# Kernel optimization log

Hardware: AMD Instinct MI355X
Metric: run time of the kernel (lower is better)

Reference implementation:

```python
import jax, jax.numpy as jnp
import numpy as np

B, S, D = 16, 1024, 768

def setup_inputs() -> dict:
    key = jax.random.key(0)
    k1, k2, k3, k4 = jax.random.split(key, 4)
    head = jax.random.normal(k1, (B, S, D), dtype=jnp.float32)
    dep = jax.random.normal(k2, (B, S, D), dtype=jnp.float32)
    edge_W = jax.random.normal(k3, (1, 2 * D), dtype=jnp.float32)
    edge_b = jax.random.normal(k4, (1,), dtype=jnp.float32)
    return {"head": head, "dep": dep, "edge_W": edge_W, "edge_b": edge_b}

def reference(head, dep, edge_W, edge_b):
    # Original: scores[b,i,j] = edge_W @ concat(head[b,i], dep[b,j]) + edge_b
    # Separable: split W into head-half and dep-half, broadcast-add over grid.
    d = head.shape[-1]
    w_h = edge_W[0, :d]   # [D]
    w_d = edge_W[0, d:]   # [D]
    s_h = jnp.einsum('bid,d->bi', head, w_h)  # [B,S]
    s_d = jnp.einsum('bjd,d->bj', dep, w_d)   # [B,S]
    return s_h[:, :, None] + s_d[:, None, :] + edge_b[0]  # [B,S,S]
```

## Files before the change

kernel.cpp:

```cpp
#include <hip/hip_runtime.h>
#include <hip/hip_bf16.h>


#define B_SZ 16
#define S_SZ 1024
#define D_SZ 768
#define ROWS (B_SZ * S_SZ)

typedef float fx4 __attribute__((ext_vector_type(4)));

__global__ __launch_bounds__(256) void dots_kernel(
    const float* __restrict__ head,
    const float* __restrict__ dep,
    const float* __restrict__ edge_W,
    float* __restrict__ s)
{
    const int gw   = (blockIdx.x * 256 + threadIdx.x) >> 6;
    const int lane = threadIdx.x & 63;
    const int is_dep = gw >> 12;
    const int base   = (gw & 4095) << 2;

    const float* __restrict__ src = is_dep ? dep : head;
    const fx4* __restrict__ wv =
        reinterpret_cast<const fx4*>(edge_W + (is_dep ? D_SZ : 0));

    const fx4 w0 = wv[lane], w1 = wv[lane + 64], w2 = wv[lane + 128];

    float acc[4];
#pragma unroll
    for (int k = 0; k < 4; ++k) {
        const fx4* __restrict__ p =
            reinterpret_cast<const fx4*>(src + (size_t)(base + k) * D_SZ);
        fx4 a0 = p[lane], a1 = p[lane + 64], a2 = p[lane + 128];
        acc[k] = a0.x * w0.x + a0.y * w0.y + a0.z * w0.z + a0.w * w0.w
               + a1.x * w1.x + a1.y * w1.y + a1.z * w1.z + a1.w * w1.w
               + a2.x * w2.x + a2.y * w2.y + a2.z * w2.z + a2.w * w2.w;
    }

#pragma unroll
    for (int k = 0; k < 4; ++k)
#pragma unroll
        for (int off = 32; off; off >>= 1)
            acc[k] += __shfl_down(acc[k], off, 64);

    if (lane == 0) {
        fx4 o; o.x = acc[0]; o.y = acc[1]; o.z = acc[2]; o.w = acc[3];
        *reinterpret_cast<fx4*>(s + (is_dep ? ROWS : 0) + base) = o;
    }
}

__global__ __launch_bounds__(256) void bcast_kernel(
    const float* __restrict__ s,
    const float* __restrict__ edge_b,
    float* __restrict__ out)
{
    const int row0 = blockIdx.x << 4;
    const int b    = row0 >> 10;

    fx4 sd = reinterpret_cast<const fx4*>(s + ROWS + ((size_t)b << 10))[threadIdx.x];
    const float bias = edge_b[0];
    sd.x += bias; sd.y += bias; sd.z += bias; sd.w += bias;

#pragma unroll
    for (int k = 0; k < 16; ++k) {
        const float sh = s[row0 + k];
        fx4 o;
        o.x = sh + sd.x;
        o.y = sh + sd.y;
        o.z = sh + sd.z;
        o.w = sh + sd.w;
        fx4* dst = reinterpret_cast<fx4*>(out + ((size_t)(row0 + k) << 10));
        __builtin_nontemporal_store(o, &dst[threadIdx.x]);
    }
}

extern "C" void kernel_launch(void* const* d_in, const int* in_sizes, int n_in,
                              void* d_out, int out_size, void* d_ws, size_t ws_size,
                              hipStream_t stream) {
    const float* head   = (const float*)d_in[0];
    const float* dep    = (const float*)d_in[1];
    const float* edge_W = (const float*)d_in[2];
    const float* edge_b = (const float*)d_in[3];
    float* out = (float*)d_out;
    float* s   = (float*)d_ws;

    dots_kernel<<<2048, 256, 0, stream>>>(head, dep, edge_W, s);
    bcast_kernel<<<ROWS / 16, 256, 0, stream>>>(s, edge_b, out);
}
```

Baseline: 31.82 us.

## Fuse head dot products into broadcast kernel, keep separate dep dot kernel

Moves the head-row dot products out of the first kernel and into the broadcast kernel. Each block now computes its 16 head scores into shared memory before writing its output rows. The first kernel shrinks to the dep half only, and the broadcast kernel no longer round-trips the head scores through the workspace. The cost is that the broadcast kernel now reads head (about 50 MB) before storing, plus a block-wide sync, which may lengthen its critical path.

```diff
diff --git a/kernel.cpp b/kernel.cpp
--- a/kernel.cpp
+++ b/kernel.cpp
@@ -9,28 +9,23 @@
 
 typedef float fx4 __attribute__((ext_vector_type(4)));
 
-__global__ __launch_bounds__(256) void dots_kernel(
-    const float* __restrict__ head,
+__global__ __launch_bounds__(256) void dep_dots_kernel(
     const float* __restrict__ dep,
     const float* __restrict__ edge_W,
-    float* __restrict__ s)
+    float* __restrict__ s_d)
 {
     const int gw   = (blockIdx.x * 256 + threadIdx.x) >> 6;
     const int lane = threadIdx.x & 63;
-    const int is_dep = gw >> 12;
-    const int base   = (gw & 4095) << 2;
+    const int base = gw << 2;
 
-    const float* __restrict__ src = is_dep ? dep : head;
-    const fx4* __restrict__ wv =
-        reinterpret_cast<const fx4*>(edge_W + (is_dep ? D_SZ : 0));
-
+    const fx4* __restrict__ wv = reinterpret_cast<const fx4*>(edge_W + D_SZ);
     const fx4 w0 = wv[lane], w1 = wv[lane + 64], w2 = wv[lane + 128];
 
     float acc[4];
 #pragma unroll
     for (int k = 0; k < 4; ++k) {
         const fx4* __restrict__ p =
-            reinterpret_cast<const fx4*>(src + (size_t)(base + k) * D_SZ);
+            reinterpret_cast<const fx4*>(dep + (size_t)(base + k) * D_SZ);
         fx4 a0 = p[lane], a1 = p[lane + 64], a2 = p[lane + 128];
         acc[k] = a0.x * w0.x + a0.y * w0.y + a0.z * w0.z + a0.w * w0.w
                + a1.x * w1.x + a1.y * w1.y + a1.z * w1.z + a1.w * w1.w
@@ -45,30 +40,62 @@
 
     if (lane == 0) {
         fx4 o; o.x = acc[0]; o.y = acc[1]; o.z = acc[2]; o.w = acc[3];
-        *reinterpret_cast<fx4*>(s + (is_dep ? ROWS : 0) + base) = o;
+        *reinterpret_cast<fx4*>(s_d + base) = o;
     }
 }
 
-__global__ __launch_bounds__(256) void bcast_kernel(
-    const float* __restrict__ s,
+__global__ __launch_bounds__(256) void head_bcast_kernel(
+    const float* __restrict__ head,
+    const float* __restrict__ s_d,
+    const float* __restrict__ edge_W,
     const float* __restrict__ edge_b,
     float* __restrict__ out)
 {
     const int row0 = blockIdx.x << 4;
     const int b    = row0 >> 10;
+    const int wave = threadIdx.x >> 6;
+    const int lane = threadIdx.x & 63;
 
-    fx4 sd = reinterpret_cast<const fx4*>(s + ROWS + ((size_t)b << 10))[threadIdx.x];
+    __shared__ float sh[16];
+
+    {
+        const fx4* __restrict__ wv = reinterpret_cast<const fx4*>(edge_W);
+        const fx4 w0 = wv[lane], w1 = wv[lane + 64], w2 = wv[lane + 128];
+        const int base = row0 + (wave << 2);
+        float acc[4];
+#pragma unroll
+        for (int k = 0; k < 4; ++k) {
+            const fx4* __restrict__ p =
+                reinterpret_cast<const fx4*>(head + (size_t)(base + k) * D_SZ);
+            fx4 a0 = p[lane], a1 = p[lane + 64], a2 = p[lane + 128];
+            acc[k] = a0.x * w0.x + a0.y * w0.y + a0.z * w0.z + a0.w * w0.w
+                   + a1.x * w1.x + a1.y * w1.y + a1.z * w1.z + a1.w * w1.w
+                   + a2.x * w2.x + a2.y * w2.y + a2.z * w2.z + a2.w * w2.w;
+        }
+#pragma unroll
+        for (int k = 0; k < 4; ++k)
+#pragma unroll
+            for (int off = 32; off; off >>= 1)
+                acc[k] += __shfl_down(acc[k], off, 64);
+        if (lane == 0) {
+#pragma unroll
+            for (int k = 0; k < 4; ++k) sh[(wave << 2) + k] = acc[k];
+        }
+    }
+    __syncthreads();
+
+    fx4 sd = reinterpret_cast<const fx4*>(s_d + ((size_t)b << 10))[threadIdx.x];
     const float bias = edge_b[0];
     sd.x += bias; sd.y += bias; sd.z += bias; sd.w += bias;
 
 #pragma unroll
     for (int k = 0; k < 16; ++k) {
-        const float sh = s[row0 + k];
+        const float h = sh[k];
         fx4 o;
-        o.x = sh + sd.x;
-        o.y = sh + sd.y;
-        o.z = sh + sd.z;
-        o.w = sh + sd.w;
+        o.x = h + sd.x;
+        o.y = h + sd.y;
+        o.z = h + sd.z;
+        o.w = h + sd.w;
         fx4* dst = reinterpret_cast<fx4*>(out + ((size_t)(row0 + k) << 10));
         __builtin_nontemporal_store(o, &dst[threadIdx.x]);
     }
@@ -82,8 +109,8 @@
     const float* edge_W = (const float*)d_in[2];
     const float* edge_b = (const float*)d_in[3];
     float* out = (float*)d_out;
-    float* s   = (float*)d_ws;
+    float* s_d = (float*)d_ws;
 
-    dots_kernel<<<2048, 256, 0, stream>>>(head, dep, edge_W, s);
-    bcast_kernel<<<ROWS / 16, 256, 0, stream>>>(s, edge_b, out);
+    dep_dots_kernel<<<ROWS / 4 / 4, 256, 0, stream>>>(dep, edge_W, s_d);
+    head_bcast_kernel<<<ROWS / 16, 256, 0, stream>>>(head, s_d, edge_W, edge_b, out);
 }
```

Measured after the change: 30.59 us. -3.9%, faster.
